# Performance work log

Measured on AMD Instinct MI355X. Metric: run time of the kernel, lower is better.

Reference implementation:

```python
import jax, jax.numpy as jnp
import numpy as np

N_NODES = 50000


def _gcn_norm(edge_index, num_nodes):
    # Add self-loops, compute symmetric normalization D^-1/2 (A+I) D^-1/2
    loops = jnp.arange(num_nodes, dtype=edge_index.dtype)
    row = jnp.concatenate([edge_index[0], loops])  # source
    col = jnp.concatenate([edge_index[1], loops])  # target
    deg = jax.ops.segment_sum(jnp.ones_like(col, dtype=jnp.float32), col,
                              num_segments=num_nodes)
    dinv = jnp.where(deg > 0, jax.lax.rsqrt(deg), 0.0)
    norm = dinv[row] * dinv[col]  # [E + N]
    return row, col, norm


def _gcn_conv(x, W, b, row, col, norm, num_nodes):
    h = x @ W                              # [N, F_out] small GEMM first (as in PyG)
    msg = h[row] * norm[:, None]           # gather + scale  [E+N, F_out]
    out = jax.ops.segment_sum(msg, col, num_segments=num_nodes)  # scatter-add
    return out + b


def setup_inputs() -> dict:
    key = jax.random.key(0)
    k = jax.random.split(key, 6)
    enc_in, hidden = 128, 16
    x = jax.random.normal(k[0], (N_NODES, enc_in), dtype=jnp.float32)
    edge_index = jax.random.randint(k[1], (2, 600000), 0, N_NODES, dtype=jnp.int64)
    # Glorot-ish init for weights
    W1 = jax.random.normal(k[2], (enc_in, hidden), dtype=jnp.float32) * (1.0 / np.sqrt(enc_in))
    b1 = jnp.zeros((hidden,), dtype=jnp.float32)
    W2 = jax.random.normal(k[3], (hidden, enc_in), dtype=jnp.float32) * (1.0 / np.sqrt(hidden))
    b2 = jnp.zeros((enc_in,), dtype=jnp.float32)
    return {"x": x, "edge_index": edge_index, "W1": W1, "b1": b1, "W2": W2, "b2": b2}


def reference(x, edge_index, W1, b1, W2, b2):
    row, col, norm = _gcn_norm(edge_index, N_NODES)
    h = _gcn_conv(x, W1, b1, row, col, norm, N_NODES)
    h = jax.nn.relu(h)
    # dropout is identity in eval mode
    h = _gcn_conv(h, W2, b2, row, col, norm, N_NODES)
    return jax.nn.log_softmax(h, axis=1)
```

## Files before the change

### kernel.cpp

```cpp
#include <hip/hip_runtime.h>

#define NN 50000
#define FIN 128
#define FH 16
#define CAP 64

__global__ void k_zero_int(int* __restrict__ p, int n) {
    int i = blockIdx.x * blockDim.x + threadIdx.x;
    if (i < n) p[i] = 0;
}

__global__ void k_build(const int* __restrict__ row, const int* __restrict__ col,
                        int* __restrict__ cnt, int* __restrict__ slot, int E) {
    int e = blockIdx.x * blockDim.x + threadIdx.x;
    if (e >= E) return;
    int r = row[e], c = col[e];
    int pos = atomicAdd(&cnt[c], 1);
    if (pos < CAP) slot[c * CAP + pos] = r;
}

__global__ void k_dinv(const int* __restrict__ cnt, float* __restrict__ dinv, int n) {
    int i = blockIdx.x * blockDim.x + threadIdx.x;
    if (i < n) dinv[i] = rsqrtf((float)cnt[i] + 1.0f);
}

__global__ __launch_bounds__(256) void k_gemm1(const float* __restrict__ x,
                                               const float* __restrict__ W1,
                                               const float* __restrict__ dinv,
                                               float* __restrict__ g1, int n) {
    int i = blockIdx.x * blockDim.x + threadIdx.x;
    if (i >= n) return;
    float acc[FH];
#pragma unroll
    for (int j = 0; j < FH; ++j) acc[j] = 0.f;
    const float4* xr = (const float4*)(x + (size_t)i * FIN);
#pragma unroll 4
    for (int kk = 0; kk < FIN / 4; ++kk) {
        float4 xv = xr[kk];
        const float* w = W1 + kk * 4 * FH;
#pragma unroll
        for (int j = 0; j < FH; ++j)
            acc[j] += xv.x * w[j] + xv.y * w[FH + j] + xv.z * w[2 * FH + j] + xv.w * w[3 * FH + j];
    }
    float d = dinv[i];
    float4* o = (float4*)(g1 + (size_t)i * FH);
#pragma unroll
    for (int q = 0; q < 4; ++q)
        o[q] = make_float4(acc[4 * q] * d, acc[4 * q + 1] * d, acc[4 * q + 2] * d, acc[4 * q + 3] * d);
}

__global__ __launch_bounds__(256) void k_agg1(const float* __restrict__ g1,
                                              const int* __restrict__ cnt,
                                              const int* __restrict__ slot,
                                              const float* __restrict__ dinv,
                                              const float* __restrict__ b1,
                                              float* __restrict__ g2, int n4) {
    int gid = blockIdx.x * blockDim.x + threadIdx.x;
    if (gid >= n4) return;
    int i = gid >> 2, q = gid & 3;
    float4 s = ((const float4*)g1)[gid];
    int d = cnt[i];
    if (d > CAP) d = CAP;
    const int* sl = slot + i * CAP;
    for (int e = 0; e < d; ++e) {
        int r = sl[e];
        float4 gv = ((const float4*)g1)[r * 4 + q];
        s.x += gv.x; s.y += gv.y; s.z += gv.z; s.w += gv.w;
    }
    float di = dinv[i];
    const float* bb = b1 + q * 4;
    float4 o;
    o.x = fmaxf(s.x * di + bb[0], 0.f) * di;
    o.y = fmaxf(s.y * di + bb[1], 0.f) * di;
    o.z = fmaxf(s.z * di + bb[2], 0.f) * di;
    o.w = fmaxf(s.w * di + bb[3], 0.f) * di;
    ((float4*)g2)[gid] = o;
}

__global__ __launch_bounds__(256) void k_agg2(const float* __restrict__ g2,
                                              const int* __restrict__ cnt,
                                              const int* __restrict__ slot,
                                              const float* __restrict__ dinv,
                                              float* __restrict__ v2, int n4) {
    int gid = blockIdx.x * blockDim.x + threadIdx.x;
    if (gid >= n4) return;
    int i = gid >> 2, q = gid & 3;
    float4 s = ((const float4*)g2)[gid];
    int d = cnt[i];
    if (d > CAP) d = CAP;
    const int* sl = slot + i * CAP;
    for (int e = 0; e < d; ++e) {
        int r = sl[e];
        float4 gv = ((const float4*)g2)[r * 4 + q];
        s.x += gv.x; s.y += gv.y; s.z += gv.z; s.w += gv.w;
    }
    float di = dinv[i];
    ((float4*)v2)[gid] = make_float4(s.x * di, s.y * di, s.z * di, s.w * di);
}

__global__ __launch_bounds__(256) void k_final(const float* __restrict__ v2,
                                               const float* __restrict__ W2,
                                               const float* __restrict__ b2,
                                               float* __restrict__ out, int n) {
    int wave = threadIdx.x >> 6, lane = threadIdx.x & 63;
    int nd = blockIdx.x * 4 + wave;
    if (nd >= n) return;
    const float* v = v2 + (size_t)nd * FH;
    float vv[FH];
#pragma unroll
    for (int k = 0; k < FH; ++k) vv[k] = v[k];
    float y0 = b2[lane], y1 = b2[lane + 64];
#pragma unroll
    for (int k = 0; k < FH; ++k) {
        y0 += vv[k] * W2[k * FIN + lane];
        y1 += vv[k] * W2[k * FIN + 64 + lane];
    }
    float m = fmaxf(y0, y1);
#pragma unroll
    for (int o = 32; o; o >>= 1) m = fmaxf(m, __shfl_xor(m, o));
    float s = __expf(y0 - m) + __expf(y1 - m);
#pragma unroll
    for (int o = 32; o; o >>= 1) s += __shfl_xor(s, o);
    float ls = m + logf(s);
    out[(size_t)nd * FIN + lane] = y0 - ls;
    out[(size_t)nd * FIN + 64 + lane] = y1 - ls;
}

extern "C" void kernel_launch(void* const* d_in, const int* in_sizes, int n_in,
                              void* d_out, int out_size, void* d_ws, size_t ws_size,
                              hipStream_t stream) {
    const float* x  = (const float*)d_in[0];
    const int*   ei = (const int*)d_in[1];
    const float* W1 = (const float*)d_in[2];
    const float* b1 = (const float*)d_in[3];
    const float* W2 = (const float*)d_in[4];
    const float* b2 = (const float*)d_in[5];
    float* out = (float*)d_out;

    const int N = NN;
    const int E = in_sizes[1] / 2;
    const int* row = ei;
    const int* col = ei + E;

    int*   cnt  = (int*)d_ws;
    float* dinv = (float*)d_ws + 50000;
    float* g1   = (float*)d_ws + 100000;
    float* g2   = (float*)d_ws + 900000;
    float* v2   = (float*)d_ws + 1700000;
    int*   slot = (int*)d_ws + 2500000;

    hipLaunchKernelGGL(k_zero_int, dim3((N + 255) / 256), dim3(256), 0, stream, cnt, N);
    hipLaunchKernelGGL(k_build, dim3((E + 255) / 256), dim3(256), 0, stream, row, col, cnt, slot, E);
    hipLaunchKernelGGL(k_dinv, dim3((N + 255) / 256), dim3(256), 0, stream, cnt, dinv, N);
    hipLaunchKernelGGL(k_gemm1, dim3((N + 255) / 256), dim3(256), 0, stream, x, W1, dinv, g1, N);
    hipLaunchKernelGGL(k_agg1, dim3((N * 4 + 255) / 256), dim3(256), 0, stream, g1, cnt, slot, dinv, b1, g2, N * 4);
    hipLaunchKernelGGL(k_agg2, dim3((N * 4 + 255) / 256), dim3(256), 0, stream, g2, cnt, slot, dinv, v2, N * 4);
    hipLaunchKernelGGL(k_final, dim3((N + 3) / 4), dim3(256), 0, stream, v2, W2, b2, out, N);
}
```

Measured before the change: 184.2 us.

## Fuse dinv into GEMM, aggregation 2 into final, unroll agg1 gathers

Folds the degree-normalisation kernel into the first GEMM and replaces the zero kernel with a memset. It also fuses the second aggregation with the output GEMM and log-softmax: one wave per node splits edges across four lane groups and reduces with shuffles. The first aggregation loop is unrolled by four so more independent gathers are in flight. Together these drop three launches and the v2 intermediate round-trip, but the fused kernel keeps one wave per node, which may leave lanes idle on low-degree nodes.

```diff
diff --git a/kernel.cpp b/kernel.cpp
--- a/kernel.cpp
+++ b/kernel.cpp
@@ -4,11 +4,6 @@
 #define FIN 128
 #define FH 16
 #define CAP 64
-
-__global__ void k_zero_int(int* __restrict__ p, int n) {
-    int i = blockIdx.x * blockDim.x + threadIdx.x;
-    if (i < n) p[i] = 0;
-}
 
 __global__ void k_build(const int* __restrict__ row, const int* __restrict__ col,
                         int* __restrict__ cnt, int* __restrict__ slot, int E) {
@@ -19,14 +14,10 @@
     if (pos < CAP) slot[c * CAP + pos] = r;
 }
 
-__global__ void k_dinv(const int* __restrict__ cnt, float* __restrict__ dinv, int n) {
-    int i = blockIdx.x * blockDim.x + threadIdx.x;
-    if (i < n) dinv[i] = rsqrtf((float)cnt[i] + 1.0f);
-}
-
 __global__ __launch_bounds__(256) void k_gemm1(const float* __restrict__ x,
                                                const float* __restrict__ W1,
-                                               const float* __restrict__ dinv,
+                                               const int* __restrict__ cnt,
+                                               float* __restrict__ dinv,
                                                float* __restrict__ g1, int n) {
     int i = blockIdx.x * blockDim.x + threadIdx.x;
     if (i >= n) return;
@@ -42,7 +33,8 @@
         for (int j = 0; j < FH; ++j)
             acc[j] += xv.x * w[j] + xv.y * w[FH + j] + xv.z * w[2 * FH + j] + xv.w * w[3 * FH + j];
     }
-    float d = dinv[i];
+    float d = rsqrtf((float)cnt[i] + 1.0f);
+    dinv[i] = d;
     float4* o = (float4*)(g1 + (size_t)i * FH);
 #pragma unroll
     for (int q = 0; q < 4; ++q)
@@ -62,10 +54,21 @@
     int d = cnt[i];
     if (d > CAP) d = CAP;
     const int* sl = slot + i * CAP;
-    for (int e = 0; e < d; ++e) {
-        int r = sl[e];
-        float4 gv = ((const float4*)g1)[r * 4 + q];
-        s.x += gv.x; s.y += gv.y; s.z += gv.z; s.w += gv.w;
+    int e = 0;
+    for (; e + 4 <= d; e += 4) {
+        int r0 = sl[e], r1 = sl[e + 1], r2 = sl[e + 2], r3 = sl[e + 3];
+        float4 a0 = ((const float4*)g1)[r0 * 4 + q];
+        float4 a1 = ((const float4*)g1)[r1 * 4 + q];
+        float4 a2 = ((const float4*)g1)[r2 * 4 + q];
+        float4 a3 = ((const float4*)g1)[r3 * 4 + q];
+        s.x += (a0.x + a1.x) + (a2.x + a3.x);
+        s.y += (a0.y + a1.y) + (a2.y + a3.y);
+        s.z += (a0.z + a1.z) + (a2.z + a3.z);
+        s.w += (a0.w + a1.w) + (a2.w + a3.w);
+    }
+    for (; e < d; ++e) {
+        float4 a = ((const float4*)g1)[sl[e] * 4 + q];
+        s.x += a.x; s.y += a.y; s.z += a.z; s.w += a.w;
     }
     float di = dinv[i];
     const float* bb = b1 + q * 4;
@@ -77,38 +80,32 @@
     ((float4*)g2)[gid] = o;
 }
 
-__global__ __launch_bounds__(256) void k_agg2(const float* __restrict__ g2,
-                                              const int* __restrict__ cnt,
-                                              const int* __restrict__ slot,
-                                              const float* __restrict__ dinv,
-                                              float* __restrict__ v2, int n4) {
-    int gid = blockIdx.x * blockDim.x + threadIdx.x;
-    if (gid >= n4) return;
-    int i = gid >> 2, q = gid & 3;
-    float4 s = ((const float4*)g2)[gid];
-    int d = cnt[i];
-    if (d > CAP) d = CAP;
-    const int* sl = slot + i * CAP;
-    for (int e = 0; e < d; ++e) {
-        int r = sl[e];
-        float4 gv = ((const float4*)g2)[r * 4 + q];
-        s.x += gv.x; s.y += gv.y; s.z += gv.z; s.w += gv.w;
-    }
-    float di = dinv[i];
-    ((float4*)v2)[gid] = make_float4(s.x * di, s.y * di, s.z * di, s.w * di);
-}
-
-__global__ __launch_bounds__(256) void k_final(const float* __restrict__ v2,
-                                               const float* __restrict__ W2,
-                                               const float* __restrict__ b2,
-                                               float* __restrict__ out, int n) {
+__global__ __launch_bounds__(256) void k_agg2final(const float* __restrict__ g2,
+                                                   const int* __restrict__ cnt,
+                                                   const int* __restrict__ slot,
+                                                   const float* __restrict__ dinv,
+                                                   const float* __restrict__ W2,
+                                                   const float* __restrict__ b2,
+                                                   float* __restrict__ out, int n) {
     int wave = threadIdx.x >> 6, lane = threadIdx.x & 63;
     int nd = blockIdx.x * 4 + wave;
     if (nd >= n) return;
-    const float* v = v2 + (size_t)nd * FH;
+    int f = lane & 15, grp = lane >> 4;
+    int d = cnt[nd];
+    if (d > CAP) d = CAP;
+    const int* sl = slot + nd * CAP;
+    float p = 0.f;
+    for (int e = grp; e < d; e += 4) {
+        int r = sl[e];
+        p += g2[r * FH + f];
+    }
+    p += __shfl_xor(p, 16);
+    p += __shfl_xor(p, 32);
+    p += g2[nd * FH + f];
+    p *= dinv[nd];
     float vv[FH];
 #pragma unroll
-    for (int k = 0; k < FH; ++k) vv[k] = v[k];
+    for (int k = 0; k < FH; ++k) vv[k] = __shfl(p, k);
     float y0 = b2[lane], y1 = b2[lane + 64];
 #pragma unroll
     for (int k = 0; k < FH; ++k) {
@@ -146,14 +143,11 @@
     float* dinv = (float*)d_ws + 50000;
     float* g1   = (float*)d_ws + 100000;
     float* g2   = (float*)d_ws + 900000;
-    float* v2   = (float*)d_ws + 1700000;
-    int*   slot = (int*)d_ws + 2500000;
+    int*   slot = (int*)d_ws + 1700000;
 
-    hipLaunchKernelGGL(k_zero_int, dim3((N + 255) / 256), dim3(256), 0, stream, cnt, N);
+    hipMemsetAsync(cnt, 0, N * sizeof(int), stream);
     hipLaunchKernelGGL(k_build, dim3((E + 255) / 256), dim3(256), 0, stream, row, col, cnt, slot, E);
-    hipLaunchKernelGGL(k_dinv, dim3((N + 255) / 256), dim3(256), 0, stream, cnt, dinv, N);
-    hipLaunchKernelGGL(k_gemm1, dim3((N + 255) / 256), dim3(256), 0, stream, x, W1, dinv, g1, N);
+    hipLaunchKernelGGL(k_gemm1, dim3((N + 255) / 256), dim3(256), 0, stream, x, W1, cnt, dinv, g1, N);
     hipLaunchKernelGGL(k_agg1, dim3((N * 4 + 255) / 256), dim3(256), 0, stream, g1, cnt, slot, dinv, b1, g2, N * 4);
-    hipLaunchKernelGGL(k_agg2, dim3((N * 4 + 255) / 256), dim3(256), 0, stream, g2, cnt, slot, dinv, v2, N * 4);
-    hipLaunchKernelGGL(k_final, dim3((N + 3) / 4), dim3(256), 0, stream, v2, W2, b2, out, N);
+    hipLaunchKernelGGL(k_agg2final, dim3((N + 3) / 4), dim3(256), 0, stream, g2, cnt, slot, dinv, W2, b2, out, N);
 }
```

New measurement: 170.0 us. -7.7%, faster.
